# Kernel optimization log

Measured on AMD Instinct MI355X. Metric: run time of the kernel, lower is better.

## Reference

```python
import jax, jax.numpy as jnp
import numpy as np

D_MODEL = 512
EXPAND = 2
D_INNER = D_MODEL * EXPAND      # 1024
STATE = 64                      # N
DT_RANK = D_MODEL // 16         # 32
CONV_K = 4
K_WIN = 8                       # window of the approximate selective scan
LN_EPS = 1e-5


def setup_inputs() -> dict:
    key = jax.random.key(0)
    ks = jax.random.split(key, 8)
    norm = lambda k, shape, scale: (jax.random.normal(k, shape, jnp.float32) * scale)
    return {
        "x": jax.random.normal(ks[0], (1, 1024, D_MODEL), jnp.float32),
        "in_proj_w": norm(ks[1], (2 * D_INNER, D_MODEL), D_MODEL ** -0.5),
        "conv_w": norm(ks[2], (D_INNER, 1, CONV_K), 0.5),            # depthwise [O, I/g=1, K]
        "conv_b": jnp.zeros((D_INNER,), jnp.float32),
        "x_proj_w": norm(ks[3], (DT_RANK + 2 * STATE, D_INNER), D_INNER ** -0.5),
        "dt_proj_w": norm(ks[4], (D_INNER, DT_RANK), DT_RANK ** -0.5),
        "dt_proj_b": jnp.zeros((D_INNER,), jnp.float32),
        "A_log": jnp.broadcast_to(
            jnp.log(jnp.arange(1, STATE + 1, dtype=jnp.float32)), (D_INNER, STATE)
        ) + 0.0,
        "D_param": jnp.ones((D_INNER,), jnp.float32),
        "out_proj_w": norm(ks[5], (D_MODEL, D_INNER), D_INNER ** -0.5),
        "ln_w": jnp.ones((D_MODEL,), jnp.float32),
        "ln_b": jnp.zeros((D_MODEL,), jnp.float32),
    }


def _selective_scan(x, dt, A, Bp, Cp, Dp):
    """Windowed selective scan (faithful to the torch loop, vectorized).

    h_t = sum_{s=max(0,t-K+1)}^{t} exp(sum_{j=s+1}^{t} dt_j * A) * dt_s * B_s * x_s
    y_t = <h_t, C_t> + D * x_t
    x, dt: [B, L, d]; A: [d, N]; Bp, Cp: [B, L, N]; Dp: [d]
    """
    L = x.shape[1]
    K = min(L, K_WIN)
    log_dA = dt[..., None] * A                                # [B,L,d,N], <= 0
    dBx = dt[..., None] * Bp[:, :, None, :] * x[..., None]    # [B,L,d,N]
    cs = jnp.cumsum(log_dA, axis=1)                           # prefix sums of log-decay
    h = dBx
    for k in range(1, K):  # fixed small window, 7 iterations
        decay = jnp.exp(cs[:, k:] - cs[:, :-k])               # prod dA over (t-k, t]
        h = h.at[:, k:].add(decay * dBx[:, :-k])
    y = jnp.einsum('bldn,bln->bld', h, Cp) + Dp * x
    return y


def reference(x, in_proj_w, conv_w, conv_b, x_proj_w, dt_proj_w, dt_proj_b,
              A_log, D_param, out_proj_w, ln_w, ln_b):
    residual = x
    xz = x @ in_proj_w.T                                      # [B,L,2*d_inner]
    x_in, z = jnp.split(xz, 2, axis=-1)

    # causal depthwise conv1d (torch pads 3 both sides then keeps first L)
    xc = jnp.transpose(x_in, (0, 2, 1))                       # [B,d,L]
    xc = jax.lax.conv_general_dilated(
        xc, conv_w, window_strides=(1,), padding=[(CONV_K - 1, 0)],
        dimension_numbers=('NCH', 'OIH', 'NCH'), feature_group_count=D_INNER,
    ) + conv_b[None, :, None]
    xc = jax.nn.silu(jnp.transpose(xc, (0, 2, 1)))            # [B,L,d]

    x_dbl = xc @ x_proj_w.T                                   # [B,L,dt_rank+2N]
    dt, Bp, Cp = jnp.split(x_dbl, [DT_RANK, DT_RANK + STATE], axis=-1)
    dt = jax.nn.softplus(dt @ dt_proj_w.T + dt_proj_b)        # [B,L,d]
    A = -jnp.exp(A_log)                                       # [d,N]

    y = _selective_scan(xc, dt, A, Bp, Cp, D_param)
    y = y * jax.nn.silu(z)
    out = y @ out_proj_w.T + residual

    mu = out.mean(-1, keepdims=True)
    var = ((out - mu) ** 2).mean(-1, keepdims=True)
    return (out - mu) * jax.lax.rsqrt(var + LN_EPS) * ln_w + ln_b
```

## Files before the change

### kernel.cpp

```cpp
#include <hip/hip_runtime.h>
#include <hip/hip_fp16.h>
#include <math.h>

#define LSEQ    1024
#define DMODEL  512
#define DINNER  1024
#define NSTATE  64
#define NFUSED  1152
#define CHUNKT  32
#define PROWS   40
#define NCH     16

#define MB (1024u * 1024u)
#define XZ_OFF      (0)
#define XC_OFF      (8u * MB)
#define XCBF_OFF    (12u * MB)
#define XBF_OFF     (14u * MB)
#define INWBF_OFF   (15u * MB)
#define OUTWBF_OFF  (17u * MB)
#define WF_OFF      (18u * MB)
#define FUSED_OFF   (20u * MB + 256u * 1024)
#define BCHI_OFF    (24u * MB + 768u * 1024)
#define YBF_OFF     (25u * MB)
#define OUTPRE_OFF  (27u * MB)

typedef __attribute__((ext_vector_type(8))) short bf16x8;
typedef __attribute__((ext_vector_type(4))) float f32x4;
typedef __attribute__((ext_vector_type(2))) float f32x2;

__device__ inline unsigned short f2bf(float f) {
  unsigned int u = __float_as_uint(f);
  u += 0x7fff + ((u >> 16) & 1);
  return (unsigned short)(u >> 16);
}
__device__ inline float h2f(unsigned short h) {
  return __half2float(__ushort_as_half(h));
}
__device__ inline float fexp2(float x) { return __builtin_amdgcn_exp2f(x); }

__global__ __launch_bounds__(256) void prep_kernel(
    const float* __restrict__ x, const float* __restrict__ inw,
    const float* __restrict__ outw, const float* __restrict__ xpw,
    const float* __restrict__ dtw, unsigned short* __restrict__ x_bf,
    unsigned short* __restrict__ inw_bf, unsigned short* __restrict__ outw_bf,
    unsigned short* __restrict__ Wf) {
  const int blk = blockIdx.x;
  if (blk < 2048) {
    const int i = blk * 256 + threadIdx.x;
    const float* src;
    unsigned short* dst;
    int j;
    if (i < 131072) {
      src = x; dst = x_bf; j = i;
    } else if (i < 393216) {
      src = inw; dst = inw_bf; j = i - 131072;
    } else {
      src = outw; dst = outw_bf; j = i - 393216;
    }
    const float4 v = *(const float4*)&src[(size_t)j * 4];
    ushort4 o;
    o.x = f2bf(v.x); o.y = f2bf(v.y); o.z = f2bf(v.z); o.w = f2bf(v.w);
    *(ushort4*)&dst[(size_t)j * 4] = o;
  } else if (blk < 2176) {
    const int r = blk - 2048;
    for (int i = threadIdx.x; i < 1024; i += 256)
      Wf[(size_t)r * 1024 + i] = f2bf(xpw[(size_t)(32 + r) * 1024 + i]);
  } else {
    const int dbase = (blk - 2176) * 8;
    __shared__ float w8[8][32];
    w8[threadIdx.x >> 5][threadIdx.x & 31] =
        dtw[(size_t)(dbase + (threadIdx.x >> 5)) * 32 + (threadIdx.x & 31)];
    __syncthreads();
    for (int i = threadIdx.x; i < 1024; i += 256) {
      float xv[32];
#pragma unroll
      for (int q = 0; q < 32; ++q) xv[q] = xpw[(size_t)q * 1024 + i];
#pragma unroll
      for (int dd = 0; dd < 8; ++dd) {
        float s = 0.f;
#pragma unroll
        for (int q = 0; q < 32; ++q) s = fmaf(w8[dd][q], xv[q], s);
        Wf[(size_t)(128 + dbase + dd) * 1024 + i] = f2bf(s);
      }
    }
  }
}

template <int BM, int BN, int WM, int WN, bool RESID, bool WBCH>
__global__ __launch_bounds__(256) void gemm_bf(
    const unsigned short* __restrict__ A, const unsigned short* __restrict__ B,
    float* __restrict__ C, const float* __restrict__ resid,
    unsigned short* __restrict__ bch, int M, int N, int K) {
  constexpr int BK = 64;
  constexpr int WTM = BM / WM;
  constexpr int WTN = BN / WN;
  constexpr int FM = WTM / 16;
  constexpr int FN = WTN / 16;
  constexpr int APASS = (BM * BK * 2) / 4096;
  constexpr int BPASS = (BN * BK * 2) / 4096;

  __shared__ unsigned short As[2][BM * BK];
  __shared__ unsigned short Bs[2][BN * BK];

  const int tid = threadIdx.x;
  const int lane = tid & 63;
  const int wave = tid >> 6;
  const int wr = (wave / WN) * WTM;
  const int wc = (wave % WN) * WTN;
  const int bm = blockIdx.y * BM;
  const int bn = blockIdx.x * BN;

  auto stage = [&](int buf, int kt) {
#pragma unroll
    for (int p = 0; p < APASS; ++p) {
      const int s = tid + p * 256;
      const int row = s >> 3;
      const int sch = (s & 7) ^ (row & 7);
      const unsigned short* src = A + (size_t)(bm + row) * K + kt + sch * 8;
      __builtin_amdgcn_global_load_lds(
          (const __attribute__((address_space(1))) unsigned int*)src,
          (__attribute__((address_space(3))) unsigned int*)(&As[buf][s * 8]),
          16, 0, 0);
    }
#pragma unroll
    for (int p = 0; p < BPASS; ++p) {
      const int s = tid + p * 256;
      const int row = s >> 3;
      const int sch = (s & 7) ^ (row & 7);
      const unsigned short* src = B + (size_t)(bn + row) * K + kt + sch * 8;
      __builtin_amdgcn_global_load_lds(
          (const __attribute__((address_space(1))) unsigned int*)src,
          (__attribute__((address_space(3))) unsigned int*)(&Bs[buf][s * 8]),
          16, 0, 0);
    }
  };

  f32x4 acc[FM][FN];
#pragma unroll
  for (int m = 0; m < FM; ++m)
#pragma unroll
    for (int n = 0; n < FN; ++n) acc[m][n] = (f32x4){0.f, 0.f, 0.f, 0.f};

  const int nt = K / BK;
  stage(0, 0);
  __syncthreads();
  int cur = 0;
  for (int t = 0; t < nt; ++t) {
    if (t + 1 < nt) stage(cur ^ 1, (t + 1) * BK);
#pragma unroll
    for (int kk = 0; kk < BK / 32; ++kk) {
      bf16x8 a[FM], b[FN];
#pragma unroll
      for (int m = 0; m < FM; ++m) {
        const int arow = wr + m * 16 + (lane & 15);
        const int ach = (kk * 4 + (lane >> 4)) ^ (arow & 7);
        a[m] = *(const bf16x8*)(&As[cur][arow * BK + ach * 8]);
      }
#pragma unroll
      for (int n = 0; n < FN; ++n) {
        const int brow = wc + n * 16 + (lane & 15);
        const int bchk = (kk * 4 + (lane >> 4)) ^ (brow & 7);
        b[n] = *(const bf16x8*)(&Bs[cur][brow * BK + bchk * 8]);
      }
#pragma unroll
      for (int m = 0; m < FM; ++m)
#pragma unroll
        for (int n = 0; n < FN; ++n)
          acc[m][n] = __builtin_amdgcn_mfma_f32_16x16x32_bf16(a[m], b[n],
                                                              acc[m][n], 0, 0, 0);
    }
    __syncthreads();
    cur ^= 1;
  }

#pragma unroll
  for (int m = 0; m < FM; ++m)
#pragma unroll
    for (int n = 0; n < FN; ++n) {
      const int col = bn + wc + n * 16 + (lane & 15);
#pragma unroll
      for (int r = 0; r < 4; ++r) {
        const int row = bm + wr + m * 16 + (lane >> 4) * 4 + r;
        float v = acc[m][n][r];
        if (RESID) v += resid[(size_t)row * N + col];
        C[(size_t)row * N + col] = v;
        if (WBCH) {
          if (col < 128) {
            const int j = col & 63, hi = col >> 6;
            bch[(size_t)row * 128 + j * 2 + hi] =
                __half_as_ushort(__float2half(v));
          }
        }
      }
    }
}

__global__ __launch_bounds__(256) void conv_silu_kernel(
    const float* __restrict__ xz, const float* __restrict__ w,
    const float* __restrict__ b, float* __restrict__ xc,
    unsigned short* __restrict__ xc_bf) {
  const int idx4 = blockIdx.x * 256 + threadIdx.x;
  const int t = idx4 >> 8;
  const int d4 = (idx4 & 255) << 2;

  float4 wv[4];
#pragma unroll
  for (int dd = 0; dd < 4; ++dd) wv[dd] = *(const float4*)&w[(d4 + dd) * 4];
  const float4 bv = *(const float4*)&b[d4];
  float acc[4] = {bv.x, bv.y, bv.z, bv.w};

#pragma unroll
  for (int j = 0; j < 4; ++j) {
    const int ts = t - 3 + j;
    if (ts >= 0) {
      const float4 xv = *(const float4*)&xz[(size_t)ts * 2048 + d4];
      const float xs[4] = {xv.x, xv.y, xv.z, xv.w};
#pragma unroll
      for (int dd = 0; dd < 4; ++dd)
        acc[dd] = fmaf(xs[dd], ((const float*)&wv[dd])[j], acc[dd]);
    }
  }
  float4 o;
  ushort4 ob;
  float* op = (float*)&o;
#pragma unroll
  for (int dd = 0; dd < 4; ++dd) {
    const float s = acc[dd] / (1.f + __expf(-acc[dd]));
    op[dd] = s;
    ((unsigned short*)&ob)[dd] = f2bf(s);
  }
  *(float4*)&xc[(size_t)t * DINNER + d4] = o;
  *(ushort4*)&xc_bf[(size_t)t * DINNER + d4] = ob;
}

__global__ __launch_bounds__(512) void scan_kernel(
    const float* __restrict__ fused,
    const unsigned int* __restrict__ bchi,
    const float* __restrict__ xc,
    const float* __restrict__ xz,
    const float* __restrict__ A_log,
    const float* __restrict__ dtb,
    const float* __restrict__ Dp,
    unsigned short* __restrict__ y_bf) {
  __shared__ unsigned int bch[PROWS * 64];
  __shared__ float4 dtl4[PROWS * 8];
  __shared__ unsigned int auxl[CHUNKT * NCH];
  __shared__ unsigned short ytile[CHUNKT * NCH];

  const int tid = threadIdx.x;
  const int lane = tid & 63;
  const int wave = tid >> 6;
  const int d0 = blockIdx.x * NCH;
  const int t0 = blockIdx.y * CHUNKT;
  const int T = t0 - 8;

#pragma unroll
  for (int pp = 0; pp < 2; ++pp) {
    const int idx = pp * 512 + tid;
    if (idx < PROWS * 16) {
      const int p = idx >> 4;
      const int c4 = (idx & 15) * 4;
      const int gt = T + p;
      uint4 v = make_uint4(0u, 0u, 0u, 0u);
      if (gt >= 0) v = *(const uint4*)&bchi[(size_t)gt * 64 + c4];
      *(uint4*)&bch[p * 64 + c4] = v;
    }
  }

  if (tid < 4 * PROWS) {
    const int row = tid >> 2;
    const int dloc = (tid & 3) * 4;
    const int gt = T + row;
    if (gt >= 0) {
      const float4 f  = *(const float4*)&fused[(size_t)gt * NFUSED + 128 + d0 + dloc];
      const float4 xv = *(const float4*)&xc[(size_t)gt * DINNER + d0 + dloc];
      const float4 zv = *(const float4*)&xz[(size_t)gt * 2048 + DINNER + d0 + dloc];
      const float4 dp = *(const float4*)&Dp[d0 + dloc];
      const float4 db = *(const float4*)&dtb[d0 + dloc];
      const float fa[4] = {f.x, f.y, f.z, f.w};
      const float xa[4] = {xv.x, xv.y, xv.z, xv.w};
      const float za[4] = {zv.x, zv.y, zv.z, zv.w};
      const float pa[4] = {dp.x, dp.y, dp.z, dp.w};
      const float ba[4] = {db.x, db.y, db.z, db.w};
      float dts[4], dtxs[4];
#pragma unroll
      for (int q = 0; q < 4; ++q) {
        const float dtp = fa[q] + ba[q];
        const float dt = (dtp > 20.f) ? dtp : __logf(1.f + __expf(dtp));
        dts[q] = dt;
        dtxs[q] = dt * xa[q];
        if (row >= 8) {
          const float dxc = pa[q] * xa[q];
          const float sz = za[q] / (1.f + __expf(-za[q]));
          auxl[(row - 8) * NCH + dloc + q] =
              (unsigned int)__half_as_ushort(__float2half(dxc)) |
              ((unsigned int)__half_as_ushort(__float2half(sz)) << 16);
        }
      }
      dtl4[row * 8 + (dloc >> 1)] = make_float4(dts[0], dts[1], dtxs[0], dtxs[1]);
      dtl4[row * 8 + (dloc >> 1) + 1] = make_float4(dts[2], dts[3], dtxs[2], dtxs[3]);
    } else {
      dtl4[row * 8 + (dloc >> 1)] = make_float4(0.f, 0.f, 0.f, 0.f);
      dtl4[row * 8 + (dloc >> 1) + 1] = make_float4(0.f, 0.f, 0.f, 0.f);
    }
  }
  __syncthreads();

  const int chl = wave * 2;
  f32x2 An2v;
  An2v.x = -__expf(A_log[(size_t)(d0 + chl) * NSTATE + lane]) * 1.44269504f;
  An2v.y = -__expf(A_log[(size_t)(d0 + chl + 1) * NSTATE + lane]) * 1.44269504f;

  f32x2 ER2[8], dB2[8];
#pragma unroll
  for (int p = 0; p < 8; ++p) {
    const float4 pk = dtl4[p * 8 + wave];
    const float Bp = h2f((unsigned short)(bch[p * 64 + lane] & 0xffffu));
    f32x2 dt2; dt2.x = pk.x; dt2.y = pk.y;
    f32x2 dtx2; dtx2.x = pk.z; dtx2.y = pk.w;
    const f32x2 ea = An2v * dt2;
    f32x2 E2; E2.x = fexp2(ea.x); E2.y = fexp2(ea.y);
    f32x2 B2; B2.x = Bp; B2.y = Bp;
    ER2[p] = E2;
    dB2[p] = dtx2 * B2;
  }

  for (int sb = 0; sb < CHUNKT; sb += 8) {
#pragma unroll
    for (int qu = 0; qu < 2; ++qu) {
      float cc[8];
#pragma unroll
      for (int h4 = 0; h4 < 4; ++h4) {
        const int u = qu * 4 + h4;
        const int p = sb + 8 + u;
        const float4 pk = dtl4[p * 8 + wave];
        const unsigned int bc = bch[p * 64 + lane];
        const float Bp = h2f((unsigned short)(bc & 0xffffu));
        const float Cp = h2f((unsigned short)(bc >> 16));
        f32x2 dt2; dt2.x = pk.x; dt2.y = pk.y;
        f32x2 dtx2; dtx2.x = pk.z; dtx2.y = pk.w;
        const f32x2 ea = An2v * dt2;
        f32x2 E2; E2.x = fexp2(ea.x); E2.y = fexp2(ea.y);
        f32x2 B2; B2.x = Bp; B2.y = Bp;
        const f32x2 dBt = dtx2 * B2;

        f32x2 s2 = dB2[(u - 7) & 7];
#pragma unroll
        for (int k = 6; k >= 1; --k) {
          const int sl = (u - k) & 7;
          s2 = __builtin_elementwise_fma(ER2[sl], s2, dB2[sl]);
        }
        const f32x2 h2 = __builtin_elementwise_fma(E2, s2, dBt);
        ER2[u] = E2;
        dB2[u] = dBt;
        f32x2 Cp2; Cp2.x = Cp; Cp2.y = Cp;
        const f32x2 cc2 = h2 * Cp2;
        cc[h4 * 2] = cc2.x;
        cc[h4 * 2 + 1] = cc2.y;
      }
      float a[8];
#pragma unroll
      for (int i = 0; i < 8; ++i) a[i] = cc[i] + __shfl_xor(cc[i], 1, 64);
      float b0 = (lane & 1) ? a[1] : a[0];
      float b1 = (lane & 1) ? a[3] : a[2];
      float b2 = (lane & 1) ? a[5] : a[4];
      float b3 = (lane & 1) ? a[7] : a[6];
      b0 += __shfl_xor(b0, 2, 64);
      b1 += __shfl_xor(b1, 2, 64);
      b2 += __shfl_xor(b2, 2, 64);
      b3 += __shfl_xor(b3, 2, 64);
      float c0 = (lane & 2) ? b1 : b0;
      float c1 = (lane & 2) ? b3 : b2;
      c0 += __shfl_xor(c0, 4, 64);
      c1 += __shfl_xor(c1, 4, 64);
      float r = (lane & 4) ? c1 : c0;
      r += __shfl_xor(r, 8, 64);
      r += __shfl_xor(r, 16, 64);
      r += __shfl_xor(r, 32, 64);
      if (lane < 8) {
        const int s = sb + qu * 4 + (lane >> 1);
        const int ch = chl + (lane & 1);
        const unsigned int av = auxl[s * NCH + ch];
        const float dxc = h2f((unsigned short)(av & 0xffffu));
        const float sz  = h2f((unsigned short)(av >> 16));
        ytile[s * NCH + ch] = f2bf((r + dxc) * sz);
      }
    }
  }

  __syncthreads();
  if (tid < CHUNKT * 8) {
    const int t = tid >> 3;
    const int c2 = (tid & 7) * 2;
    const unsigned int vy = *(const unsigned int*)&ytile[t * NCH + c2];
    *(unsigned int*)&y_bf[(size_t)(t0 + t) * DINNER + d0 + c2] = vy;
  }
}

__global__ __launch_bounds__(256) void ln_kernel(
    const float* __restrict__ src, const float* __restrict__ w,
    const float* __restrict__ b, float* __restrict__ out) {
  const int t = blockIdx.x;
  const int i0 = threadIdx.x;
  const int i1 = threadIdx.x + 256;
  const float v0 = src[(size_t)t * DMODEL + i0];
  const float v1 = src[(size_t)t * DMODEL + i1];
  float s = v0 + v1;
  float q = v0 * v0 + v1 * v1;
#pragma unroll
  for (int m = 32; m; m >>= 1) {
    s += __shfl_xor(s, m, 64);
    q += __shfl_xor(q, m, 64);
  }
  __shared__ float ss[4], sq[4];
  const int wv = threadIdx.x >> 6;
  if ((threadIdx.x & 63) == 0) { ss[wv] = s; sq[wv] = q; }
  __syncthreads();
  s = ss[0] + ss[1] + ss[2] + ss[3];
  q = sq[0] + sq[1] + sq[2] + sq[3];
  const float mu = s * (1.f / 512.f);
  const float var = q * (1.f / 512.f) - mu * mu;
  const float inv = rsqrtf(var + 1e-5f);
  out[(size_t)t * DMODEL + i0] = (v0 - mu) * inv * w[i0] + b[i0];
  out[(size_t)t * DMODEL + i1] = (v1 - mu) * inv * w[i1] + b[i1];
}

extern "C" void kernel_launch(void* const* d_in, const int* in_sizes, int n_in,
                              void* d_out, int out_size, void* d_ws,
                              size_t ws_size, hipStream_t stream) {
  const float* x         = (const float*)d_in[0];
  const float* in_w      = (const float*)d_in[1];
  const float* conv_w    = (const float*)d_in[2];
  const float* conv_b    = (const float*)d_in[3];
  const float* xproj_w   = (const float*)d_in[4];
  const float* dtproj_w  = (const float*)d_in[5];
  const float* dtproj_b  = (const float*)d_in[6];
  const float* A_log     = (const float*)d_in[7];
  const float* Dp        = (const float*)d_in[8];
  const float* outproj_w = (const float*)d_in[9];
  const float* ln_w      = (const float*)d_in[10];
  const float* ln_b      = (const float*)d_in[11];
  float* out = (float*)d_out;

  char* ws = (char*)d_ws;
  float*          xz      = (float*)(ws + XZ_OFF);
  float*          xc      = (float*)(ws + XC_OFF);
  unsigned short* xc_bf   = (unsigned short*)(ws + XCBF_OFF);
  unsigned short* x_bf    = (unsigned short*)(ws + XBF_OFF);
  unsigned short* inw_bf  = (unsigned short*)(ws + INWBF_OFF);
  unsigned short* outw_bf = (unsigned short*)(ws + OUTWBF_OFF);
  unsigned short* Wf      = (unsigned short*)(ws + WF_OFF);
  float*          fused   = (float*)(ws + FUSED_OFF);
  unsigned short* bchi    = (unsigned short*)(ws + BCHI_OFF);
  unsigned short* y_bf    = (unsigned short*)(ws + YBF_OFF);
  float*          outpre  = (float*)(ws + OUTPRE_OFF);

  prep_kernel<<<2304, 256, 0, stream>>>(x, in_w, outproj_w, xproj_w, dtproj_w,
                                        x_bf, inw_bf, outw_bf, Wf);
  gemm_bf<64, 64, 2, 2, false, false>
      <<<dim3(2048 / 64, 1024 / 64), 256, 0, stream>>>(
          x_bf, inw_bf, xz, nullptr, nullptr, 1024, 2048, 512);
  conv_silu_kernel<<<1024, 256, 0, stream>>>(xz, conv_w, conv_b, xc, xc_bf);
  gemm_bf<64, 64, 2, 2, false, true>
      <<<dim3(NFUSED / 64, 1024 / 64), 256, 0, stream>>>(
          xc_bf, Wf, fused, nullptr, bchi, 1024, NFUSED, 1024);
  scan_kernel<<<dim3(DINNER / NCH, LSEQ / CHUNKT), 512, 0, stream>>>(
      fused, (const unsigned int*)bchi, xc, xz, A_log, dtproj_b, Dp, y_bf);
  gemm_bf<32, 32, 2, 2, true, false>
      <<<dim3(512 / 32, 1024 / 32), 256, 0, stream>>>(
          y_bf, outw_bf, outpre, x, nullptr, 1024, 512, 1024);
  ln_kernel<<<LSEQ, 256, 0, stream>>>(outpre, ln_w, ln_b, out);
}
```

Before: 92.24 us.

## Widen scan blocks to 32 channels with 4 channels per wave

Each scan block now covers 32 inner channels instead of 16, and each wave processes four channels rather than two. The B/C halo rows loaded into shared memory are therefore reused across twice as many channels, and the cross-lane reduction tree amortizes its shuffles over more outputs. In exchange the grid has half as many blocks and each thread holds more register state, which may reduce occupancy.

Measured after the change: 140.7 us. 1.53x slower.

```diff
diff --git a/kernel.cpp b/kernel.cpp
--- a/kernel.cpp
+++ b/kernel.cpp
@@ -9,7 +9,7 @@
 #define NFUSED  1152
 #define CHUNKT  32
 #define PROWS   40
-#define NCH     16
+#define NCH     32
 
 #define MB (1024u * 1024u)
 #define XZ_OFF      (0)
@@ -243,7 +243,7 @@
     const float* __restrict__ Dp,
     unsigned short* __restrict__ y_bf) {
   __shared__ unsigned int bch[PROWS * 64];
-  __shared__ float4 dtl4[PROWS * 8];
+  __shared__ float4 dtl4[PROWS * 16];
   __shared__ unsigned int auxl[CHUNKT * NCH];
   __shared__ unsigned short ytile[CHUNKT * NCH];
 
@@ -267,9 +267,9 @@
     }
   }
 
-  if (tid < 4 * PROWS) {
-    const int row = tid >> 2;
-    const int dloc = (tid & 3) * 4;
+  if (tid < 8 * PROWS) {
+    const int row = tid >> 3;
+    const int dloc = (tid & 7) * 4;
     const int gt = T + row;
     if (gt >= 0) {
       const float4 f  = *(const float4*)&fused[(size_t)gt * NFUSED + 128 + d0 + dloc];
@@ -297,89 +297,113 @@
               ((unsigned int)__half_as_ushort(__float2half(sz)) << 16);
         }
       }
-      dtl4[row * 8 + (dloc >> 1)] = make_float4(dts[0], dts[1], dtxs[0], dtxs[1]);
-      dtl4[row * 8 + (dloc >> 1) + 1] = make_float4(dts[2], dts[3], dtxs[2], dtxs[3]);
+      dtl4[row * 16 + (dloc >> 1)] = make_float4(dts[0], dts[1], dtxs[0], dtxs[1]);
+      dtl4[row * 16 + (dloc >> 1) + 1] = make_float4(dts[2], dts[3], dtxs[2], dtxs[3]);
     } else {
-      dtl4[row * 8 + (dloc >> 1)] = make_float4(0.f, 0.f, 0.f, 0.f);
-      dtl4[row * 8 + (dloc >> 1) + 1] = make_float4(0.f, 0.f, 0.f, 0.f);
+      dtl4[row * 16 + (dloc >> 1)] = make_float4(0.f, 0.f, 0.f, 0.f);
+      dtl4[row * 16 + (dloc >> 1) + 1] = make_float4(0.f, 0.f, 0.f, 0.f);
     }
   }
   __syncthreads();
 
-  const int chl = wave * 2;
-  f32x2 An2v;
-  An2v.x = -__expf(A_log[(size_t)(d0 + chl) * NSTATE + lane]) * 1.44269504f;
-  An2v.y = -__expf(A_log[(size_t)(d0 + chl + 1) * NSTATE + lane]) * 1.44269504f;
-
-  f32x2 ER2[8], dB2[8];
+  const int chl = wave * 4;
+  f32x2 An01, An23;
+  An01.x = -__expf(A_log[(size_t)(d0 + chl) * NSTATE + lane]) * 1.44269504f;
+  An01.y = -__expf(A_log[(size_t)(d0 + chl + 1) * NSTATE + lane]) * 1.44269504f;
+  An23.x = -__expf(A_log[(size_t)(d0 + chl + 2) * NSTATE + lane]) * 1.44269504f;
+  An23.y = -__expf(A_log[(size_t)(d0 + chl + 3) * NSTATE + lane]) * 1.44269504f;
+
+  f32x2 ER01[8], dB01[8], ER23[8], dB23[8];
 #pragma unroll
   for (int p = 0; p < 8; ++p) {
-    const float4 pk = dtl4[p * 8 + wave];
+    const float4 pka = dtl4[p * 16 + wave * 2];
+    const float4 pkb = dtl4[p * 16 + wave * 2 + 1];
     const float Bp = h2f((unsigned short)(bch[p * 64 + lane] & 0xffffu));
-    f32x2 dt2; dt2.x = pk.x; dt2.y = pk.y;
-    f32x2 dtx2; dtx2.x = pk.z; dtx2.y = pk.w;
-    const f32x2 ea = An2v * dt2;
-    f32x2 E2; E2.x = fexp2(ea.x); E2.y = fexp2(ea.y);
     f32x2 B2; B2.x = Bp; B2.y = Bp;
-    ER2[p] = E2;
-    dB2[p] = dtx2 * B2;
+    f32x2 dta; dta.x = pka.x; dta.y = pka.y;
+    f32x2 dxa; dxa.x = pka.z; dxa.y = pka.w;
+    f32x2 dtb2; dtb2.x = pkb.x; dtb2.y = pkb.y;
+    f32x2 dxb; dxb.x = pkb.z; dxb.y = pkb.w;
+    const f32x2 ea = An01 * dta;
+    const f32x2 eb = An23 * dtb2;
+    f32x2 Ea; Ea.x = fexp2(ea.x); Ea.y = fexp2(ea.y);
+    f32x2 Eb; Eb.x = fexp2(eb.x); Eb.y = fexp2(eb.y);
+    ER01[p] = Ea; dB01[p] = dxa * B2;
+    ER23[p] = Eb; dB23[p] = dxb * B2;
   }
 
   for (int sb = 0; sb < CHUNKT; sb += 8) {
 #pragma unroll
     for (int qu = 0; qu < 2; ++qu) {
-      float cc[8];
+      float cc[16];
 #pragma unroll
       for (int h4 = 0; h4 < 4; ++h4) {
         const int u = qu * 4 + h4;
         const int p = sb + 8 + u;
-        const float4 pk = dtl4[p * 8 + wave];
+        const float4 pka = dtl4[p * 16 + wave * 2];
+        const float4 pkb = dtl4[p * 16 + wave * 2 + 1];
         const unsigned int bc = bch[p * 64 + lane];
         const float Bp = h2f((unsigned short)(bc & 0xffffu));
         const float Cp = h2f((unsigned short)(bc >> 16));
-        f32x2 dt2; dt2.x = pk.x; dt2.y = pk.y;
-        f32x2 dtx2; dtx2.x = pk.z; dtx2.y = pk.w;
-        const f32x2 ea = An2v * dt2;
-        f32x2 E2; E2.x = fexp2(ea.x); E2.y = fexp2(ea.y);
         f32x2 B2; B2.x = Bp; B2.y = Bp;
-        const f32x2 dBt = dtx2 * B2;
-
-        f32x2 s2 = dB2[(u - 7) & 7];
+        f32x2 Cp2; Cp2.x = Cp; Cp2.y = Cp;
+        f32x2 dta; dta.x = pka.x; dta.y = pka.y;
+        f32x2 dxa; dxa.x = pka.z; dxa.y = pka.w;
+        f32x2 dtb2; dtb2.x = pkb.x; dtb2.y = pkb.y;
+        f32x2 dxb; dxb.x = pkb.z; dxb.y = pkb.w;
+        const f32x2 ea = An01 * dta;
+        const f32x2 eb = An23 * dtb2;
+        f32x2 Ea; Ea.x = fexp2(ea.x); Ea.y = fexp2(ea.y);
+        f32x2 Eb; Eb.x = fexp2(eb.x); Eb.y = fexp2(eb.y);
+        const f32x2 dBa = dxa * B2;
+        const f32x2 dBb = dxb * B2;
+
+        f32x2 sa = dB01[(u - 7) & 7];
+        f32x2 sb2 = dB23[(u - 7) & 7];
 #pragma unroll
         for (int k = 6; k >= 1; --k) {
           const int sl = (u - k) & 7;
-          s2 = __builtin_elementwise_fma(ER2[sl], s2, dB2[sl]);
+          sa = __builtin_elementwise_fma(ER01[sl], sa, dB01[sl]);
+          sb2 = __builtin_elementwise_fma(ER23[sl], sb2, dB23[sl]);
         }
-        const f32x2 h2 = __builtin_elementwise_fma(E2, s2, dBt);
-        ER2[u] = E2;
-        dB2[u] = dBt;
-        f32x2 Cp2; Cp2.x = Cp; Cp2.y = Cp;
-        const f32x2 cc2 = h2 * Cp2;
-        cc[h4 * 2] = cc2.x;
-        cc[h4 * 2 + 1] = cc2.y;
-      }
-      float a[8];
-#pragma unroll
-      for (int i = 0; i < 8; ++i) a[i] = cc[i] + __shfl_xor(cc[i], 1, 64);
-      float b0 = (lane & 1) ? a[1] : a[0];
-      float b1 = (lane & 1) ? a[3] : a[2];
-      float b2 = (lane & 1) ? a[5] : a[4];
-      float b3 = (lane & 1) ? a[7] : a[6];
-      b0 += __shfl_xor(b0, 2, 64);
-      b1 += __shfl_xor(b1, 2, 64);
-      b2 += __shfl_xor(b2, 2, 64);
-      b3 += __shfl_xor(b3, 2, 64);
-      float c0 = (lane & 2) ? b1 : b0;
-      float c1 = (lane & 2) ? b3 : b2;
-      c0 += __shfl_xor(c0, 4, 64);
-      c1 += __shfl_xor(c1, 4, 64);
-      float r = (lane & 4) ? c1 : c0;
-      r += __shfl_xor(r, 8, 64);
+        const f32x2 ha = __builtin_elementwise_fma(Ea, sa, dBa);
+        const f32x2 hb = __builtin_elementwise_fma(Eb, sb2, dBb);
+        ER01[u] = Ea; dB01[u] = dBa;
+        ER23[u] = Eb; dB23[u] = dBb;
+        const f32x2 ca = ha * Cp2;
+        const f32x2 cb = hb * Cp2;
+        cc[h4 * 4 + 0] = ca.x;
+        cc[h4 * 4 + 1] = ca.y;
+        cc[h4 * 4 + 2] = cb.x;
+        cc[h4 * 4 + 3] = cb.y;
+      }
+      float a[16];
+#pragma unroll
+      for (int i = 0; i < 16; ++i) a[i] = cc[i] + __shfl_xor(cc[i], 1, 64);
+      float b[8];
+#pragma unroll
+      for (int j = 0; j < 8; ++j) {
+        b[j] = (lane & 1) ? a[2 * j + 1] : a[2 * j];
+        b[j] += __shfl_xor(b[j], 2, 64);
+      }
+      float c[4];
+#pragma unroll
+      for (int j = 0; j < 4; ++j) {
+        c[j] = (lane & 2) ? b[2 * j + 1] : b[2 * j];
+        c[j] += __shfl_xor(c[j], 4, 64);
+      }
+      float e[2];
+#pragma unroll
+      for (int j = 0; j < 2; ++j) {
+        e[j] = (lane & 4) ? c[2 * j + 1] : c[2 * j];
+        e[j] += __shfl_xor(e[j], 8, 64);
+      }
+      float r = (lane & 8) ? e[1] : e[0];
       r += __shfl_xor(r, 16, 64);
       r += __shfl_xor(r, 32, 64);
-      if (lane < 8) {
-        const int s = sb + qu * 4 + (lane >> 1);
-        const int ch = chl + (lane & 1);
+      if (lane < 16) {
+        const int s = sb + qu * 4 + (lane >> 2);
+        const int ch = chl + (lane & 3);
         const unsigned int av = auxl[s * NCH + ch];
         const float dxc = h2f((unsigned short)(av & 0xffffu));
         const float sz  = h2f((unsigned short)(av >> 16));
@@ -389,9 +413,9 @@
   }
 
   __syncthreads();
-  if (tid < CHUNKT * 8) {
-    const int t = tid >> 3;
-    const int c2 = (tid & 7) * 2;
+  {
+    const int t = tid >> 4;
+    const int c2 = (tid & 15) * 2;
     const unsigned int vy = *(const unsigned int*)&ytile[t * NCH + c2];
     *(unsigned int*)&y_bf[(size_t)(t0 + t) * DINNER + d0 + c2] = vy;
   }
```
